# Optimization experiments

Measured on AMD Instinct MI355X. Metric: run time of the kernel, lower is better.

Reference implementation:

```python
import jax, jax.numpy as jnp
import numpy as np

B = 256       # batch
H = 512       # latent_size == hidden_size == t_channels == o_channels
O_LEN = 512   # decode steps (output_shape[0])


def setup_inputs() -> dict:
    key = jax.random.key(0)
    ks = jax.random.split(key, 7)
    s = 1.0 / np.sqrt(H)
    u = lambda k, shp: jax.random.uniform(k, shp, jnp.float32, -s, s)
    return {
        "z": jax.random.normal(ks[0], (B, H), jnp.float32),
        "W_ih": u(ks[1], (4 * H, H)),   # PyTorch LSTM weight_ih_l0, gate order i,f,g,o
        "W_hh": u(ks[2], (4 * H, H)),
        "b_ih": u(ks[3], (4 * H,)),
        "b_hh": u(ks[4], (4 * H,)),
        "W_last": u(ks[5], (H, H)),     # nn.Linear(hidden_size, o_channels)
        "b_last": u(ks[6], (H,)),
    }


def reference(z, W_ih, W_hh, b_ih, b_hh, W_last, b_last):
    b = b_ih + b_hh

    def step(carry, _):
        x, h, c = carry  # each (B, H)
        gates = x @ W_ih.T + h @ W_hh.T + b  # (B, 4H)
        i, f, g, o = jnp.split(gates, 4, axis=-1)
        c = jax.nn.sigmoid(f) * c + jax.nn.sigmoid(i) * jnp.tanh(g)
        h = jax.nn.sigmoid(o) * jnp.tanh(c)
        y = h @ W_last.T + b_last  # (B, H) -> fed back as next input
        return (y, h, c), y

    # state = (z, z) as (h0, c0); first input x0 = z
    _, ys = jax.lax.scan(step, (z, z, z), None, length=O_LEN)  # ys: (O_LEN, B, H)
    return jnp.transpose(ys, (1, 0, 2))  # (B, O_LEN, H)
```

## Files before the change

kernel.cpp:

```cpp
#include <hip/hip_runtime.h>


#define HH 512
#define TT 512

typedef _Float16 half8 __attribute__((ext_vector_type(8)));
typedef float f32x4 __attribute__((ext_vector_type(4)));

__device__ __forceinline__ float sigm(float x) { return 1.0f / (1.0f + __expf(-x)); }
__device__ __forceinline__ float tanh_(float x) { return 1.0f - 2.0f / (__expf(2.0f * x) + 1.0f); }
__device__ __forceinline__ unsigned short f16b(float x) {
    _Float16 h = (_Float16)x;
    return __builtin_bit_cast(unsigned short, h);
}

__global__ __launch_bounds__(256) void k_weff(const float* __restrict__ Wih,
                                              const float* __restrict__ Whh,
                                              const float* __restrict__ Wlast,
                                              unsigned short* __restrict__ Wbig) {
    __shared__ float wih[16 * 512];
    const int tid = threadIdx.x;
    const int r0 = blockIdx.x * 16;
    for (int i = tid; i < (16 * 512) / 4; i += 256) {
        ((float4*)wih)[i] = ((const float4*)(Wih + (size_t)r0 * 512))[i];
    }
    __syncthreads();
    float acc0[16], acc1[16];
#pragma unroll
    for (int rr = 0; rr < 16; ++rr) { acc0[rr] = 0.f; acc1[rr] = 0.f; }
    const int k0 = tid * 2;
    for (int j = 0; j < 512; ++j) {
        const float2 wl = *(const float2*)(Wlast + (size_t)j * 512 + k0);
#pragma unroll
        for (int rr = 0; rr < 16; ++rr) {
            const float a = wih[rr * 512 + j];
            acc0[rr] += a * wl.x;
            acc1[rr] += a * wl.y;
        }
    }
#pragma unroll
    for (int rr = 0; rr < 16; ++rr) {
        const int gr = r0 + rr;
        const int q = gr >> 9, j = gr & 511;
        const int dst = 80 * (j >> 4) + q * 16 + (j & 15);
        const float v0 = acc0[rr] + Whh[(size_t)gr * 512 + k0];
        const float v1 = acc1[rr] + Whh[(size_t)gr * 512 + k0 + 1];
        Wbig[(size_t)dst * 512 + k0] = f16b(v0);
        Wbig[(size_t)dst * 512 + k0 + 1] = f16b(v1);
    }
}

__global__ __launch_bounds__(256) void k_pack(const float* __restrict__ z,
                                              const float* __restrict__ Wih,
                                              const float* __restrict__ Whh,
                                              const float* __restrict__ bih,
                                              const float* __restrict__ bhh,
                                              const float* __restrict__ Wlast,
                                              const float* __restrict__ blast,
                                              unsigned short* __restrict__ Wbig,
                                              unsigned short* __restrict__ W0big,
                                              float* __restrict__ biasEff,
                                              float* __restrict__ bias0,
                                              unsigned short* __restrict__ hbuf,
                                              unsigned int* __restrict__ counters) {
    const int nthr = gridDim.x * blockDim.x;
    const int gtid = blockIdx.x * blockDim.x + threadIdx.x;
    for (int e = gtid; e < 2560 * 512; e += nthr) {
        const int r = e >> 9, k = e & 511;
        const int s = r / 80, rem = r - s * 80;
        const int tau = rem >> 4, jj = rem & 15;
        const int j = s * 16 + jj;
        if (tau == 4) {
            const unsigned short v = f16b(Wlast[(size_t)j * 512 + k]);
            Wbig[e] = v;
            W0big[e] = v;
        } else {
            const int gr = tau * 512 + j;
            W0big[e] = f16b(Wih[(size_t)gr * 512 + k] + Whh[(size_t)gr * 512 + k]);
        }
    }
    for (int r = gtid; r < 2560; r += nthr) {
        const int s = r / 80, rem = r - s * 80;
        const int tau = rem >> 4, jj = rem & 15;
        const int j = s * 16 + jj;
        if (tau == 4) {
            bias0[r] = blast[j];
            biasEff[r] = blast[j];
        } else {
            const int gr = tau * 512 + j;
            const float base = bih[gr] + bhh[gr];
            float dot = 0.f;
            for (int k = 0; k < 512; ++k) dot += Wih[(size_t)gr * 512 + k] * blast[k];
            bias0[r] = base;
            biasEff[r] = base + dot;
        }
    }
    for (int e = gtid; e < 256 * 512; e += nthr) {
        const int b = e >> 9, k = e & 511;
        const int g = b >> 5, bl = b & 31;
        hbuf[((size_t)(g * 2) * 32 + bl) * 512 + k] = f16b(z[e]);
    }
    for (int e = gtid; e < 512; e += nthr) counters[e] = 0u;
}

__global__ __launch_bounds__(256, 1) void k_lstm(const unsigned short* __restrict__ Wbig,
                                                 const unsigned short* __restrict__ W0big,
                                                 const float* __restrict__ biasEff,
                                                 const float* __restrict__ bias0,
                                                 unsigned short* __restrict__ hbuf,
                                                 unsigned int* __restrict__ counters,
                                                 const float* __restrict__ z,
                                                 float* __restrict__ out) {
    const int g = blockIdx.x & 7;
    const int pair = blockIdx.x >> 3;
    const int tid = threadIdx.x;
    const int wave = tid >> 6;
    const int lane = tid & 63;
    const int l15 = lane & 15;
    const int q4 = lane >> 4;

    __shared__ unsigned short hstage[32 * 520];
    __shared__ float gatesL[2 * 32 * 68];
    __shared__ float cL[2 * 32 * 18];

    const int sl = wave >> 1;
    const int slice = 2 * pair + sl;
    const int ntile0 = (wave & 1) ? 3 : 0;
    const int ntcount = (wave & 1) ? 2 : 3;

    unsigned short* hb0 = hbuf + (size_t)(g * 2) * 32 * 512;
    unsigned short* hb1 = hb0 + 32 * 512;
    unsigned int* cnt = counters + g * 64;

    for (int idx = tid; idx < 1024; idx += 256) {
        const int s2 = idx >> 9;
        const int b = (idx >> 4) & 31, jj = idx & 15;
        cL[(s2 * 32 + b) * 18 + jj] =
            z[(size_t)(g * 32 + b) * 512 + 16 * (2 * pair + s2) + jj];
    }

    half8 bfrag[3][16];
#pragma unroll
    for (int tt = 0; tt < 3; ++tt) {
        if (tt < ntcount) {
            const int row = 80 * slice + (ntile0 + tt) * 16 + l15;
#pragma unroll
            for (int kk = 0; kk < 16; ++kk) {
                bfrag[tt][kk] = *(const half8*)(W0big + (size_t)row * 512 + kk * 32 + q4 * 8);
            }
        }
    }
    float bias0v[3], biasEv[3];
#pragma unroll
    for (int tt = 0; tt < 3; ++tt) {
        if (tt < ntcount) {
            const int r = 80 * slice + (ntile0 + tt) * 16 + l15;
            bias0v[tt] = bias0[r];
            biasEv[tt] = biasEff[r];
        } else {
            bias0v[tt] = 0.f;
            biasEv[tt] = 0.f;
        }
    }

    for (int t = 0; t <= 512; ++t) {
        {
            const unsigned short* src = (t & 1) ? hb1 : hb0;
            const char* p = (const char*)src + tid * 16;
            half8 st[8];
            asm volatile(
                "global_load_dwordx4 %0, %8, off sc0 sc1\n\t"
                "global_load_dwordx4 %1, %9, off sc0 sc1\n\t"
                "global_load_dwordx4 %2, %10, off sc0 sc1\n\t"
                "global_load_dwordx4 %3, %11, off sc0 sc1\n\t"
                "global_load_dwordx4 %4, %12, off sc0 sc1\n\t"
                "global_load_dwordx4 %5, %13, off sc0 sc1\n\t"
                "global_load_dwordx4 %6, %14, off sc0 sc1\n\t"
                "global_load_dwordx4 %7, %15, off sc0 sc1\n\t"
                "s_waitcnt vmcnt(0)"
                : "=&v"(st[0]), "=&v"(st[1]), "=&v"(st[2]), "=&v"(st[3]),
                  "=&v"(st[4]), "=&v"(st[5]), "=&v"(st[6]), "=&v"(st[7])
                : "v"(p), "v"(p + 4096), "v"(p + 8192), "v"(p + 12288),
                  "v"(p + 16384), "v"(p + 20480), "v"(p + 24576), "v"(p + 28672)
                : "memory");
#pragma unroll
            for (int i = 0; i < 8; ++i) {
                const int ci = i * 256 + tid;
                const int row = ci >> 6, col = ci & 63;
                *(half8*)(hstage + row * 520 + col * 8) = st[i];
            }
        }
        __syncthreads();

        f32x4 acc[3][2];
#pragma unroll
        for (int tt = 0; tt < 3; ++tt) {
            const float bv = (t == 0) ? bias0v[tt] : biasEv[tt];
            acc[tt][0] = (f32x4){bv, bv, bv, bv};
            acc[tt][1] = (f32x4){bv, bv, bv, bv};
        }
#pragma unroll
        for (int kk = 0; kk < 16; ++kk) {
            const half8 a0 = *(const half8*)(hstage + (l15)*520 + kk * 32 + q4 * 8);
            const half8 a1 = *(const half8*)(hstage + (16 + l15) * 520 + kk * 32 + q4 * 8);
#pragma unroll
            for (int tt = 0; tt < 3; ++tt) {
                if (tt < ntcount) {
                    acc[tt][0] = __builtin_amdgcn_mfma_f32_16x16x32_f16(a0, bfrag[tt][kk], acc[tt][0], 0, 0, 0);
                    acc[tt][1] = __builtin_amdgcn_mfma_f32_16x16x32_f16(a1, bfrag[tt][kk], acc[tt][1], 0, 0, 0);
                }
            }
        }

        if ((wave & 1) && t >= 1) {
            const int n = 16 * slice + l15;
#pragma unroll
            for (int mt = 0; mt < 2; ++mt) {
#pragma unroll
                for (int r = 0; r < 4; ++r) {
                    const int m = mt * 16 + q4 * 4 + r;
                    const size_t off = (size_t)(g * 32 + m) * (TT * HH) + (size_t)(t - 1) * HH + n;
                    out[off] = acc[1][mt][r];
                }
            }
        }
        if (t == 512) break;

        {
            const int nst = (wave & 1) ? 1 : 3;
#pragma unroll
            for (int tt = 0; tt < 3; ++tt) {
                if (tt < nst) {
                    const int col = (ntile0 + tt) * 16 + l15;
#pragma unroll
                    for (int mt = 0; mt < 2; ++mt) {
#pragma unroll
                        for (int r = 0; r < 4; ++r) {
                            const int m = mt * 16 + q4 * 4 + r;
                            gatesL[(sl * 32 + m) * 68 + col] = acc[tt][mt][r];
                        }
                    }
                }
            }
        }
        __syncthreads();

        {
            const int b = tid >> 3, jp = tid & 7;
            const int j0 = jp * 2;
            unsigned short* dst = (t & 1) ? hb0 : hb1;
#pragma unroll
            for (int s2 = 0; s2 < 2; ++s2) {
                const float* gb = gatesL + (s2 * 32 + b) * 68;
                const float2 iv = *(const float2*)(gb + j0);
                const float2 fvv = *(const float2*)(gb + 16 + j0);
                const float2 gv = *(const float2*)(gb + 32 + j0);
                const float2 ov = *(const float2*)(gb + 48 + j0);
                float2 cv = *(const float2*)(cL + (s2 * 32 + b) * 18 + j0);
                const float c0 = sigm(fvv.x) * cv.x + sigm(iv.x) * tanh_(gv.x);
                const float c1 = sigm(fvv.y) * cv.y + sigm(iv.y) * tanh_(gv.y);
                const float h0 = sigm(ov.x) * tanh_(c0);
                const float h1 = sigm(ov.y) * tanh_(c1);
                cv.x = c0;
                cv.y = c1;
                *(float2*)(cL + (s2 * 32 + b) * 18 + j0) = cv;
                const unsigned int packed =
                    (unsigned int)f16b(h0) | ((unsigned int)f16b(h1) << 16);
                __hip_atomic_store(
                    (unsigned int*)(dst + b * 512 + 16 * (2 * pair + s2) + j0), packed,
                    __ATOMIC_RELAXED, __HIP_MEMORY_SCOPE_AGENT);
            }
        }

        if (t == 0) {
#pragma unroll
            for (int tt = 0; tt < 3; ++tt) {
                if (tt < ntcount) {
                    const int row = 80 * slice + (ntile0 + tt) * 16 + l15;
#pragma unroll
                    for (int kk = 0; kk < 16; ++kk) {
                        bfrag[tt][kk] = *(const half8*)(Wbig + (size_t)row * 512 + kk * 32 + q4 * 8);
                    }
                }
            }
        }

        __syncthreads();
        if (tid == 0) {
            __hip_atomic_fetch_add(cnt, 1u, __ATOMIC_RELAXED, __HIP_MEMORY_SCOPE_AGENT);
            const unsigned int target = 16u * (unsigned)(t + 1);
            int guard = 0;
            while (__hip_atomic_load(cnt, __ATOMIC_RELAXED, __HIP_MEMORY_SCOPE_AGENT) < target &&
                   ++guard < 65536) {
            }
        }
        __syncthreads();
    }
}

extern "C" void kernel_launch(void* const* d_in, const int* in_sizes, int n_in,
                              void* d_out, int out_size, void* d_ws, size_t ws_size,
                              hipStream_t stream) {
    const float* z = (const float*)d_in[0];
    const float* Wih = (const float*)d_in[1];
    const float* Whh = (const float*)d_in[2];
    const float* bih = (const float*)d_in[3];
    const float* bhh = (const float*)d_in[4];
    const float* Wlast = (const float*)d_in[5];
    const float* blast = (const float*)d_in[6];
    float* out = (float*)d_out;

    char* ws = (char*)d_ws;
    unsigned short* Wbig = (unsigned short*)(ws);
    unsigned short* W0big = (unsigned short*)(ws + 2621440);
    float* biasEff = (float*)(ws + 5242880);
    float* bias0 = (float*)(ws + 5253120);
    unsigned short* hbuf = (unsigned short*)(ws + 5263360);
    unsigned int* counters = (unsigned int*)(ws + 5787648);

    k_weff<<<128, 256, 0, stream>>>(Wih, Whh, Wlast, Wbig);
    k_pack<<<512, 256, 0, stream>>>(z, Wih, Whh, bih, bhh, Wlast, blast, Wbig, W0big, biasEff,
                                    bias0, hbuf, counters);
    k_lstm<<<128, 256, 0, stream>>>(Wbig, W0big, biasEff, bias0, hbuf, counters, z, out);
}
```

Baseline: 2.106 ms.

## Replace atomic counter barrier with per-wave flag stores and ballot polling

Replaces the per-group atomic fetch_add counter barrier with per-wave flag words that each wave stores directly. One wave polls all 64 flags of its group with a single load per lane plus a ballot. The output store is moved after the flag publication so it overlaps the wait, and __syncthreads is replaced by a lighter barrier that waits only on LDS counters. The aim is to cut the serialized atomic traffic and barrier latency on the per-step critical path. The correctness of cross-block visibility now rests on the sc0 sc1 stores and the vmcnt wait ordering.

```diff
diff --git a/kernel.cpp b/kernel.cpp
--- a/kernel.cpp
+++ b/kernel.cpp
@@ -6,6 +6,13 @@
 
 typedef _Float16 half8 __attribute__((ext_vector_type(8)));
 typedef float f32x4 __attribute__((ext_vector_type(4)));
+
+#define BAR()                                              \
+    do {                                                   \
+        asm volatile("s_waitcnt lgkmcnt(0)" ::: "memory"); \
+        __builtin_amdgcn_s_barrier();                      \
+        asm volatile("" ::: "memory");                     \
+    } while (0)
 
 __device__ __forceinline__ float sigm(float x) { return 1.0f / (1.0f + __expf(-x)); }
 __device__ __forceinline__ float tanh_(float x) { return 1.0f - 2.0f / (__expf(2.0f * x) + 1.0f); }
@@ -62,7 +69,7 @@
                                               float* __restrict__ biasEff,
                                               float* __restrict__ bias0,
                                               unsigned short* __restrict__ hbuf,
-                                              unsigned int* __restrict__ counters) {
+                                              unsigned int* __restrict__ flags) {
     const int nthr = gridDim.x * blockDim.x;
     const int gtid = blockIdx.x * blockDim.x + threadIdx.x;
     for (int e = gtid; e < 2560 * 512; e += nthr) {
@@ -100,7 +107,7 @@
         const int g = b >> 5, bl = b & 31;
         hbuf[((size_t)(g * 2) * 32 + bl) * 512 + k] = f16b(z[e]);
     }
-    for (int e = gtid; e < 512; e += nthr) counters[e] = 0u;
+    for (int e = gtid; e < 512; e += nthr) flags[e] = 0u;
 }
 
 __global__ __launch_bounds__(256, 1) void k_lstm(const unsigned short* __restrict__ Wbig,
@@ -108,7 +115,7 @@
                                                  const float* __restrict__ biasEff,
                                                  const float* __restrict__ bias0,
                                                  unsigned short* __restrict__ hbuf,
-                                                 unsigned int* __restrict__ counters,
+                                                 unsigned int* __restrict__ flags,
                                                  const float* __restrict__ z,
                                                  float* __restrict__ out) {
     const int g = blockIdx.x & 7;
@@ -130,7 +137,7 @@
 
     unsigned short* hb0 = hbuf + (size_t)(g * 2) * 32 * 512;
     unsigned short* hb1 = hb0 + 32 * 512;
-    unsigned int* cnt = counters + g * 64;
+    unsigned int* fgrp = flags + g * 64;
 
     for (int idx = tid; idx < 1024; idx += 256) {
         const int s2 = idx >> 9;
@@ -162,6 +169,8 @@
             biasEv[tt] = 0.f;
         }
     }
+
+    __syncthreads();
 
     for (int t = 0; t <= 512; ++t) {
         {
@@ -190,7 +199,7 @@
                 *(half8*)(hstage + row * 520 + col * 8) = st[i];
             }
         }
-        __syncthreads();
+        BAR();
 
         f32x4 acc[3][2];
 #pragma unroll
@@ -212,19 +221,22 @@
             }
         }
 
-        if ((wave & 1) && t >= 1) {
-            const int n = 16 * slice + l15;
-#pragma unroll
-            for (int mt = 0; mt < 2; ++mt) {
-#pragma unroll
-                for (int r = 0; r < 4; ++r) {
-                    const int m = mt * 16 + q4 * 4 + r;
-                    const size_t off = (size_t)(g * 32 + m) * (TT * HH) + (size_t)(t - 1) * HH + n;
-                    out[off] = acc[1][mt][r];
-                }
-            }
-        }
-        if (t == 512) break;
+        if (t == 512) {
+            if (wave & 1) {
+                const int n = 16 * slice + l15;
+#pragma unroll
+                for (int mt = 0; mt < 2; ++mt) {
+#pragma unroll
+                    for (int r = 0; r < 4; ++r) {
+                        const int m = mt * 16 + q4 * 4 + r;
+                        const size_t off =
+                            (size_t)(g * 32 + m) * (TT * HH) + (size_t)(t - 1) * HH + n;
+                        out[off] = acc[1][mt][r];
+                    }
+                }
+            }
+            break;
+        }
 
         {
             const int nst = (wave & 1) ? 1 : 3;
@@ -243,7 +255,7 @@
                 }
             }
         }
-        __syncthreads();
+        BAR();
 
         {
             const int b = tid >> 3, jp = tid & 7;
@@ -266,9 +278,9 @@
                 *(float2*)(cL + (s2 * 32 + b) * 18 + j0) = cv;
                 const unsigned int packed =
                     (unsigned int)f16b(h0) | ((unsigned int)f16b(h1) << 16);
-                __hip_atomic_store(
-                    (unsigned int*)(dst + b * 512 + 16 * (2 * pair + s2) + j0), packed,
-                    __ATOMIC_RELAXED, __HIP_MEMORY_SCOPE_AGENT);
+                unsigned int* pp = (unsigned int*)(dst + b * 512 + 16 * (2 * pair + s2) + j0);
+                asm volatile("global_store_dword %0, %1, off sc0 sc1" ::"v"(pp), "v"(packed)
+                             : "memory");
             }
         }
 
@@ -285,16 +297,41 @@
             }
         }
 
-        __syncthreads();
-        if (tid == 0) {
-            __hip_atomic_fetch_add(cnt, 1u, __ATOMIC_RELAXED, __HIP_MEMORY_SCOPE_AGENT);
-            const unsigned int target = 16u * (unsigned)(t + 1);
-            int guard = 0;
-            while (__hip_atomic_load(cnt, __ATOMIC_RELAXED, __HIP_MEMORY_SCOPE_AGENT) < target &&
-                   ++guard < 65536) {
-            }
-        }
-        __syncthreads();
+        asm volatile("s_waitcnt vmcnt(0)" ::: "memory");
+        if (lane == 0) {
+            unsigned int* fp = fgrp + pair * 4 + wave;
+            const unsigned int fv = (unsigned int)t + 1u;
+            asm volatile("global_store_dword %0, %1, off sc0 sc1" ::"v"(fp), "v"(fv)
+                         : "memory");
+        }
+
+        if ((wave & 1) && t >= 1) {
+            const int n = 16 * slice + l15;
+#pragma unroll
+            for (int mt = 0; mt < 2; ++mt) {
+#pragma unroll
+                for (int r = 0; r < 4; ++r) {
+                    const int m = mt * 16 + q4 * 4 + r;
+                    const size_t off =
+                        (size_t)(g * 32 + m) * (TT * HH) + (size_t)(t - 1) * HH + n;
+                    out[off] = acc[1][mt][r];
+                }
+            }
+        }
+
+        if (wave == 0) {
+            const unsigned int* fp = fgrp + lane;
+            const unsigned int tgt = (unsigned int)t + 1u;
+            unsigned int pv;
+            int gd = 0;
+            do {
+                asm volatile("global_load_dword %0, %1, off sc0 sc1\n\ts_waitcnt vmcnt(0)"
+                             : "=v"(pv)
+                             : "v"(fp)
+                             : "memory");
+            } while (__ballot(pv >= tgt) != ~0ull && ++gd < 65536);
+        }
+        BAR();
     }
 }
 
@@ -316,10 +353,10 @@
     float* biasEff = (float*)(ws + 5242880);
     float* bias0 = (float*)(ws + 5253120);
     unsigned short* hbuf = (unsigned short*)(ws + 5263360);
-    unsigned int* counters = (unsigned int*)(ws + 5787648);
+    unsigned int* flags = (unsigned int*)(ws + 5787648);
 
     k_weff<<<128, 256, 0, stream>>>(Wih, Whh, Wlast, Wbig);
     k_pack<<<512, 256, 0, stream>>>(z, Wih, Whh, bih, bhh, Wlast, blast, Wbig, W0big, biasEff,
-                                    bias0, hbuf, counters);
-    k_lstm<<<128, 256, 0, stream>>>(Wbig, W0big, biasEff, bias0, hbuf, counters, z, out);
-}
+                                    bias0, hbuf, flags);
+    k_lstm<<<128, 256, 0, stream>>>(Wbig, W0big, biasEff, bias0, hbuf, flags, z, out);
+}
```

Measured after the change: 3.393 ms. 1.61x slower.
